# Kernel tuning notes

Measured on AMD Instinct MI355X. Metric: run time of the kernel, lower is better.

The kernel has to match this reference:

```python
import jax, jax.numpy as jnp
import numpy as np

N = 100000      # entities per graph
DIM = 128       # embedding / GAT dim
NHEADS = 2
NLAYER = 2
DH = DIM // NHEADS
DEG = 16        # avg in-degree
B = 4096        # alignment batch
ALPHA = 0.2     # LeakyReLU slope


def _make_edges(k):
    # random sources, uniform in-degree DEG per destination, plus self-loops
    src = jax.random.randint(k, (N * DEG,), 0, N)
    dst = jnp.repeat(jnp.arange(N), DEG)
    loop = jnp.arange(N)
    return jnp.stack([jnp.concatenate([src, loop]),
                      jnp.concatenate([dst, loop])]).astype(jnp.int32)


def setup_inputs() -> dict:
    key = jax.random.key(0)
    ks = jax.random.split(key, 9)
    emb_sr = jax.random.normal(ks[0], (N, DIM), jnp.float32) * 0.1
    emb_tg = jax.random.normal(ks[1], (N, DIM), jnp.float32) * 0.1
    edges_sr = _make_edges(ks[2])
    edges_tg = _make_edges(ks[3])
    Ws = jax.random.normal(ks[4], (NLAYER, NHEADS, DIM, DH), jnp.float32) / np.float32(np.sqrt(DIM))
    a_src = jax.random.normal(ks[5], (NLAYER, NHEADS, DH), jnp.float32) * 0.1
    a_dst = jax.random.normal(ks[6], (NLAYER, NHEADS, DH), jnp.float32) * 0.1
    sr_data = jax.random.randint(ks[7], (B,), 0, N)
    tg_data = jax.random.randint(ks[8], (B,), 0, N)
    return {"emb_sr": emb_sr, "emb_tg": emb_tg, "Ws": Ws, "a_src": a_src,
            "a_dst": a_dst, "edges_sr": edges_sr, "edges_tg": edges_tg,
            "sr_data": sr_data, "tg_data": tg_data}


def _gat(x, edges, Ws, a_src, a_dst):
    src, dst = edges[0], edges[1]
    for l in range(NLAYER):
        h = jnp.einsum('nd,hde->nhe', x, Ws[l])              # [N,H,DH]
        es = jnp.einsum('nhe,he->nh', h, a_src[l])           # [N,H]
        ed = jnp.einsum('nhe,he->nh', h, a_dst[l])           # [N,H]
        e = jax.nn.leaky_relu(es[src] + ed[dst], ALPHA)      # [E,H]
        m = jax.ops.segment_max(e, dst, num_segments=N)      # per-dst softmax
        w = jnp.exp(e - m[dst])
        denom = jax.ops.segment_sum(w, dst, num_segments=N)
        coef = w / (denom[dst] + 1e-16)                      # [E,H]
        out = jax.ops.segment_sum(coef[:, :, None] * h[src], dst, num_segments=N)
        out = out.reshape(N, NHEADS * DH)                    # concat heads
        x = jax.nn.elu(out) if l < NLAYER - 1 else out
    return x


def reference(emb_sr, emb_tg, Ws, a_src, a_dst, edges_sr, edges_tg, sr_data, tg_data):
    g_sr = _gat(emb_sr, edges_sr, Ws, a_src, a_dst)
    g_tg = _gat(emb_tg, edges_tg, Ws, a_src, a_dst)
    return g_sr[sr_data], g_tg[tg_data]
```

## Files before the change

kernel.cpp:

```cpp
#include <hip/hip_runtime.h>
#include <math.h>


#define N_NODES 100000
#define DIM     128
#define DH      64
#define DEG     16
#define BATCH   4096

typedef unsigned int   uint32;
typedef unsigned short u16;

typedef __attribute__((ext_vector_type(8))) short bf16x8;
typedef __attribute__((ext_vector_type(4))) float f32x4;

static __device__ __forceinline__ u16 bf16rne(float a) {
    uint32 ua = __float_as_uint(a);
    ua = (ua + 0x7FFFu + ((ua >> 16) & 1u)) >> 16;
    return (u16)ua;
}
static __device__ __forceinline__ uint32 bf2pack(float a, float b) {
    uint32 ua = __float_as_uint(a), ub = __float_as_uint(b);
    ua = (ua + 0x7FFFu + ((ua >> 16) & 1u)) >> 16;
    ub = (ub + 0x7FFFu + ((ub >> 16) & 1u)) >> 16;
    return (ub << 16) | (ua & 0xFFFFu);
}

__global__ void wfrag_init(const float* __restrict__ Ws, u16* __restrict__ wfrag) {
    const int l = blockIdx.x;
    for (int i = threadIdx.x; i < 16384; i += 256) {
        const int j = i & 7, lane = (i >> 3) & 63, nt = (i >> 9) & 7, ks = i >> 12;
        const int d = ks * 32 + (lane >> 4) * 8 + j;
        const int c = nt * 16 + (lane & 15);
        const float v = Ws[(size_t)(((l * 2 + (c >> 6)) * DIM) + d) * DH + (c & 63)];
        wfrag[l * 16384 + i] = bf16rne(v);
    }
}

template <bool BF16IN>
__global__ __launch_bounds__(256) void gat_transform_mfma(
    const void* __restrict__ xa, const void* __restrict__ xb,
    const u16* __restrict__ wfrag,
    const float* __restrict__ a_src,
    const float* __restrict__ a_dst,
    u16* __restrict__ hb,
    float* __restrict__ es,
    float* __restrict__ ed)
{
    __shared__ u16 xsh[64][136];

    const int g = blockIdx.y;
    const size_t row0 = (size_t)blockIdx.x * 64;
    const int t = threadIdx.x;

    if (BF16IN) {
        const u16* __restrict__ x = (const u16*)(g ? xb : xa);
        #pragma unroll
        for (int i = 0; i < 4; ++i) {
            const int c = i * 256 + t;
            const int r = c >> 4, col = (c & 15) * 8;
            const size_t gr = row0 + r;
            uint4 v = make_uint4(0u, 0u, 0u, 0u);
            if (gr < N_NODES) v = *(const uint4*)(x + gr * DIM + col);
            *(uint4*)&xsh[r][col] = v;
        }
    } else {
        const float* __restrict__ x = (const float*)(g ? xb : xa);
        #pragma unroll
        for (int i = 0; i < 8; ++i) {
            const int c = i * 256 + t;
            const int r = c >> 5, col = (c & 31) * 4;
            const size_t gr = row0 + r;
            float4 v = make_float4(0.f, 0.f, 0.f, 0.f);
            if (gr < N_NODES) v = *(const float4*)(x + gr * DIM + col);
            uint2 pk; pk.x = bf2pack(v.x, v.y); pk.y = bf2pack(v.z, v.w);
            *(uint2*)&xsh[r][col] = pk;
        }
    }
    __syncthreads();

    const int w = t >> 6, l = t & 63;
    const int wrow = w * 16;
    const int cl = l & 15, kg = l >> 4;

    f32x4 acc[8];
    #pragma unroll
    for (int nt = 0; nt < 8; ++nt) acc[nt] = (f32x4){0.f, 0.f, 0.f, 0.f};

    #pragma unroll
    for (int ks = 0; ks < 4; ++ks) {
        const bf16x8 a = *(const bf16x8*)&xsh[wrow + cl][ks * 32 + kg * 8];
        const u16* wp = wfrag + ks * 4096 + l * 8;
        #pragma unroll
        for (int nt = 0; nt < 8; ++nt) {
            const bf16x8 b = *(const bf16x8*)(wp + nt * 512);
            acc[nt] = __builtin_amdgcn_mfma_f32_16x16x32_bf16(a, b, acc[nt], 0, 0, 0);
        }
    }

    float av0[4], av1[4], dv0[4], dv1[4];
    #pragma unroll
    for (int nt = 0; nt < 4; ++nt) {
        av0[nt] = a_src[nt * 16 + cl];
        av1[nt] = a_src[DH + nt * 16 + cl];
        dv0[nt] = a_dst[nt * 16 + cl];
        dv1[nt] = a_dst[DH + nt * 16 + cl];
    }
    float pe0[4] = {0,0,0,0}, pe1[4] = {0,0,0,0};
    float pd0[4] = {0,0,0,0}, pd1[4] = {0,0,0,0};
    #pragma unroll
    for (int r = 0; r < 4; ++r)
        #pragma unroll
        for (int nt = 0; nt < 4; ++nt) {
            pe0[r] = fmaf(acc[nt][r],     av0[nt], pe0[r]);
            pd0[r] = fmaf(acc[nt][r],     dv0[nt], pd0[r]);
            pe1[r] = fmaf(acc[nt + 4][r], av1[nt], pe1[r]);
            pd1[r] = fmaf(acc[nt + 4][r], dv1[nt], pd1[r]);
        }
    #pragma unroll
    for (int msk = 1; msk < 16; msk <<= 1)
        #pragma unroll
        for (int r = 0; r < 4; ++r) {
            pe0[r] += __shfl_xor(pe0[r], msk, 64);
            pe1[r] += __shfl_xor(pe1[r], msk, 64);
            pd0[r] += __shfl_xor(pd0[r], msk, 64);
            pd1[r] += __shfl_xor(pd1[r], msk, 64);
        }
    if (cl == 0) {
        #pragma unroll
        for (int r = 0; r < 4; ++r) {
            const size_t gr = row0 + wrow + kg * 4 + r;
            if (gr < N_NODES) {
                const size_t o = ((size_t)g * N_NODES + gr) * 2;
                es[o] = pe0[r]; es[o + 1] = pe1[r];
                ed[o] = pd0[r]; ed[o + 1] = pd1[r];
            }
        }
    }

    __syncthreads();
    #pragma unroll
    for (int nt = 0; nt < 8; ++nt)
        #pragma unroll
        for (int r = 0; r < 4; ++r)
            xsh[wrow + kg * 4 + r][nt * 16 + cl] = bf16rne(acc[nt][r]);
    __syncthreads();
    #pragma unroll
    for (int i = 0; i < 4; ++i) {
        const int c = i * 256 + t;
        const int r = c >> 4, col = (c & 15) * 8;
        const size_t gr = row0 + r;
        if (gr < N_NODES)
            *(uint4*)(hb + ((size_t)g * N_NODES + gr) * DIM + col) = *(const uint4*)&xsh[r][col];
    }
}

template <bool FINAL>
__global__ __launch_bounds__(256) void gat_aggregate(
    const int* __restrict__ edges_a, const int* __restrict__ edges_b,
    const u16* __restrict__ hb, const float* __restrict__ es,
    const float* __restrict__ ed,
    const int* __restrict__ idx_a, const int* __restrict__ idx_b,
    void* __restrict__ out, int count)
{
    const int g   = blockIdx.y;
    const int wid = blockIdx.x * 4 + (threadIdx.x >> 6);
    if (wid >= count) return;
    const int lane = threadIdx.x & 63;
    const int head = lane >> 5;

    const int n = FINAL ? (g ? idx_b[wid] : idx_a[wid]) : wid;
    const int* __restrict__ edges = g ? edges_b : edges_a;
    const u16* __restrict__ hg   = hb + (size_t)g * N_NODES * DIM;
    const float* __restrict__ esg = es + (size_t)g * N_NODES * 2;

    const float edn = ed[((size_t)g * N_NODES + n) * 2 + head];

    int s[17];
    const int4* ep = (const int4*)(edges + (size_t)n * DEG);
    int4 q0 = ep[0], q1 = ep[1], q2 = ep[2], q3 = ep[3];
    s[0]=q0.x;  s[1]=q0.y;  s[2]=q0.z;  s[3]=q0.w;
    s[4]=q1.x;  s[5]=q1.y;  s[6]=q1.z;  s[7]=q1.w;
    s[8]=q2.x;  s[9]=q2.y;  s[10]=q2.z; s[11]=q2.w;
    s[12]=q3.x; s[13]=q3.y; s[14]=q3.z; s[15]=q3.w;
    s[16]=n;

    float w[17];
    float m = -1e30f;
    #pragma unroll
    for (int j = 0; j < 17; ++j) {
        float v = esg[s[j] * 2 + head] + edn;
        v = (v >= 0.f) ? v : 0.2f * v;
        w[j] = v;
        m = fmaxf(m, v);
    }
    float denom = 0.f;
    #pragma unroll
    for (int j = 0; j < 17; ++j) { w[j] = __expf(w[j] - m); denom += w[j]; }
    const float inv = 1.f / (denom + 1e-16f);

    float2 acc = make_float2(0.f, 0.f);
    #pragma unroll
    for (int j = 0; j < 17; ++j) {
        const uint32 u = *(const uint32*)(hg + (size_t)s[j] * DIM + lane * 2);
        const float hx = __uint_as_float(u << 16);
        const float hy = __uint_as_float(u & 0xFFFF0000u);
        acc.x = fmaf(w[j], hx, acc.x);
        acc.y = fmaf(w[j], hy, acc.y);
    }
    acc.x *= inv; acc.y *= inv;

    if (FINAL) {
        float* o = (float*)out + ((size_t)g * BATCH + wid) * DIM + lane * 2;
        *(float2*)o = acc;
    } else {
        acc.x = (acc.x > 0.f) ? acc.x : (__expf(acc.x) - 1.f);
        acc.y = (acc.y > 0.f) ? acc.y : (__expf(acc.y) - 1.f);
        u16* o = (u16*)out + ((size_t)g * N_NODES + n) * DIM + lane * 2;
        *(uint32*)o = bf2pack(acc.x, acc.y);
    }
}

extern "C" void kernel_launch(void* const* d_in, const int* in_sizes, int n_in,
                              void* d_out, int out_size, void* d_ws, size_t ws_size,
                              hipStream_t stream)
{
    const float* emb_sr = (const float*)d_in[0];
    const float* emb_tg = (const float*)d_in[1];
    const float* Ws     = (const float*)d_in[2];
    const float* a_src  = (const float*)d_in[3];
    const float* a_dst  = (const float*)d_in[4];
    const int*   edg_sr = (const int*)d_in[5];
    const int*   edg_tg = (const int*)d_in[6];
    const int*   sr_idx = (const int*)d_in[7];
    const int*   tg_idx = (const int*)d_in[8];

    u16*   hb    = (u16*)d_ws;
    u16*   x1b   = hb + (size_t)2 * N_NODES * DIM;
    float* es    = (float*)(x1b + (size_t)2 * N_NODES * DIM);
    float* ed    = es + (size_t)2 * N_NODES * 2;
    u16*   wfrag = (u16*)(ed + (size_t)2 * N_NODES * 2);

    const dim3 tgrd((N_NODES + 63) / 64, 2);
    const dim3 agrd(N_NODES / 4, 2);

    wfrag_init<<<2, 256, 0, stream>>>(Ws, wfrag);

    gat_transform_mfma<false><<<tgrd, 256, 0, stream>>>(
        emb_sr, emb_tg, wfrag, a_src, a_dst, hb, es, ed);
    gat_aggregate<false><<<agrd, 256, 0, stream>>>(
        edg_sr, edg_tg, hb, es, ed, nullptr, nullptr, x1b, N_NODES);

    gat_transform_mfma<true><<<tgrd, 256, 0, stream>>>(
        x1b, x1b + (size_t)N_NODES * DIM, wfrag + 16384,
        a_src + 2 * DH, a_dst + 2 * DH, hb, es, ed);
    gat_aggregate<true><<<dim3(BATCH / 4, 2), 256, 0, stream>>>(
        edg_sr, edg_tg, hb, es, ed, sr_idx, tg_idx, d_out, BATCH);
}
```

Baseline: 345.4 us.

## Fuse layer-1 aggregation with layer-2 MFMA transform via shared memory tile

The layer-1 neighbour aggregation (softmax plus ELU) now runs inside the layer-2 transform kernel. Each block aggregates its 64 destination rows into shared memory as bf16 and then runs the MFMA projection on them. This drops one launch and the global write and read of the intermediate x1 activations. Separate h, es and ed buffers per layer avoid overwriting data that other blocks are still reading. In exchange, each wave aggregates 16 rows one after another, which means fewer waves in flight to hide gather latency, and the aggregation uses one 256-thread block per 64 rows instead of one wave per row.

```diff
diff --git a/kernel.cpp b/kernel.cpp
--- a/kernel.cpp
+++ b/kernel.cpp
@@ -37,48 +37,12 @@
     }
 }
 
-template <bool BF16IN>
-__global__ __launch_bounds__(256) void gat_transform_mfma(
-    const void* __restrict__ xa, const void* __restrict__ xb,
-    const u16* __restrict__ wfrag,
-    const float* __restrict__ a_src,
-    const float* __restrict__ a_dst,
-    u16* __restrict__ hb,
-    float* __restrict__ es,
-    float* __restrict__ ed)
-{
-    __shared__ u16 xsh[64][136];
-
-    const int g = blockIdx.y;
-    const size_t row0 = (size_t)blockIdx.x * 64;
-    const int t = threadIdx.x;
-
-    if (BF16IN) {
-        const u16* __restrict__ x = (const u16*)(g ? xb : xa);
-        #pragma unroll
-        for (int i = 0; i < 4; ++i) {
-            const int c = i * 256 + t;
-            const int r = c >> 4, col = (c & 15) * 8;
-            const size_t gr = row0 + r;
-            uint4 v = make_uint4(0u, 0u, 0u, 0u);
-            if (gr < N_NODES) v = *(const uint4*)(x + gr * DIM + col);
-            *(uint4*)&xsh[r][col] = v;
-        }
-    } else {
-        const float* __restrict__ x = (const float*)(g ? xb : xa);
-        #pragma unroll
-        for (int i = 0; i < 8; ++i) {
-            const int c = i * 256 + t;
-            const int r = c >> 5, col = (c & 31) * 4;
-            const size_t gr = row0 + r;
-            float4 v = make_float4(0.f, 0.f, 0.f, 0.f);
-            if (gr < N_NODES) v = *(const float4*)(x + gr * DIM + col);
-            uint2 pk; pk.x = bf2pack(v.x, v.y); pk.y = bf2pack(v.z, v.w);
-            *(uint2*)&xsh[r][col] = pk;
-        }
-    }
-    __syncthreads();
-
+static __device__ __forceinline__ void mfma_tile_body(
+    u16 (*xsh)[136], int t, int g, size_t row0,
+    const u16* __restrict__ wfrag, const float* __restrict__ a_src,
+    const float* __restrict__ a_dst, u16* __restrict__ hb,
+    float* __restrict__ es, float* __restrict__ ed)
+{
     const int w = t >> 6, l = t & 63;
     const int wrow = w * 16;
     const int cl = l & 15, kg = l >> 4;
@@ -155,21 +119,113 @@
     }
 }
 
-template <bool FINAL>
-__global__ __launch_bounds__(256) void gat_aggregate(
+__global__ __launch_bounds__(256) void gat_transform_mfma(
+    const float* __restrict__ xa, const float* __restrict__ xb,
+    const u16* __restrict__ wfrag,
+    const float* __restrict__ a_src, const float* __restrict__ a_dst,
+    u16* __restrict__ hb, float* __restrict__ es, float* __restrict__ ed)
+{
+    __shared__ u16 xsh[64][136];
+    const int g = blockIdx.y;
+    const size_t row0 = (size_t)blockIdx.x * 64;
+    const int t = threadIdx.x;
+
+    const float* __restrict__ x = (const float*)(g ? xb : xa);
+    #pragma unroll
+    for (int i = 0; i < 8; ++i) {
+        const int c = i * 256 + t;
+        const int r = c >> 5, col = (c & 31) * 4;
+        const size_t gr = row0 + r;
+        float4 v = make_float4(0.f, 0.f, 0.f, 0.f);
+        if (gr < N_NODES) v = *(const float4*)(x + gr * DIM + col);
+        uint2 pk; pk.x = bf2pack(v.x, v.y); pk.y = bf2pack(v.z, v.w);
+        *(uint2*)&xsh[r][col] = pk;
+    }
+    __syncthreads();
+    mfma_tile_body(xsh, t, g, row0, wfrag, a_src, a_dst, hb, es, ed);
+}
+
+__global__ __launch_bounds__(256) void gat_fused_agg_transform(
+    const int* __restrict__ edges_a, const int* __restrict__ edges_b,
+    const u16* __restrict__ h0, const float* __restrict__ es0,
+    const float* __restrict__ ed0,
+    const u16* __restrict__ wfrag,
+    const float* __restrict__ a_src, const float* __restrict__ a_dst,
+    u16* __restrict__ h1, float* __restrict__ es1, float* __restrict__ ed1)
+{
+    __shared__ u16 xsh[64][136];
+    const int g = blockIdx.y;
+    const int t = threadIdx.x;
+    const int w = t >> 6, lane = t & 63;
+    const int head = lane >> 5;
+    const size_t dst0 = (size_t)blockIdx.x * 64;
+
+    const int* __restrict__ edges = g ? edges_b : edges_a;
+    const u16* __restrict__ hg    = h0  + (size_t)g * N_NODES * DIM;
+    const float* __restrict__ esg = es0 + (size_t)g * N_NODES * 2;
+    const float* __restrict__ edg = ed0 + (size_t)g * N_NODES * 2;
+
+    for (int i = 0; i < 16; ++i) {
+        const int r = w * 16 + i;
+        const size_t n = dst0 + r;
+        uint32 pk = 0u;
+        if (n < N_NODES) {
+            int s[17];
+            const int4* ep = (const int4*)(edges + n * DEG);
+            int4 q0 = ep[0], q1 = ep[1], q2 = ep[2], q3 = ep[3];
+            s[0]=q0.x;  s[1]=q0.y;  s[2]=q0.z;  s[3]=q0.w;
+            s[4]=q1.x;  s[5]=q1.y;  s[6]=q1.z;  s[7]=q1.w;
+            s[8]=q2.x;  s[9]=q2.y;  s[10]=q2.z; s[11]=q2.w;
+            s[12]=q3.x; s[13]=q3.y; s[14]=q3.z; s[15]=q3.w;
+            s[16]=(int)n;
+
+            const float edn = edg[n * 2 + head];
+            float wgt[17];
+            float m = -1e30f;
+            #pragma unroll
+            for (int j = 0; j < 17; ++j) {
+                float v = esg[s[j] * 2 + head] + edn;
+                v = (v >= 0.f) ? v : 0.2f * v;
+                wgt[j] = v;
+                m = fmaxf(m, v);
+            }
+            float denom = 0.f;
+            #pragma unroll
+            for (int j = 0; j < 17; ++j) { wgt[j] = __expf(wgt[j] - m); denom += wgt[j]; }
+            const float inv = 1.f / (denom + 1e-16f);
+
+            float2 acc = make_float2(0.f, 0.f);
+            #pragma unroll
+            for (int j = 0; j < 17; ++j) {
+                const uint32 u = *(const uint32*)(hg + (size_t)s[j] * DIM + lane * 2);
+                acc.x = fmaf(wgt[j], __uint_as_float(u << 16), acc.x);
+                acc.y = fmaf(wgt[j], __uint_as_float(u & 0xFFFF0000u), acc.y);
+            }
+            acc.x *= inv; acc.y *= inv;
+            acc.x = (acc.x > 0.f) ? acc.x : (__expf(acc.x) - 1.f);
+            acc.y = (acc.y > 0.f) ? acc.y : (__expf(acc.y) - 1.f);
+            pk = bf2pack(acc.x, acc.y);
+        }
+        *(uint32*)&xsh[r][lane * 2] = pk;
+    }
+    __syncthreads();
+    mfma_tile_body(xsh, t, g, dst0, wfrag, a_src, a_dst, h1, es1, ed1);
+}
+
+__global__ __launch_bounds__(256) void gat_aggregate_final(
     const int* __restrict__ edges_a, const int* __restrict__ edges_b,
     const u16* __restrict__ hb, const float* __restrict__ es,
     const float* __restrict__ ed,
     const int* __restrict__ idx_a, const int* __restrict__ idx_b,
-    void* __restrict__ out, int count)
+    float* __restrict__ out)
 {
     const int g   = blockIdx.y;
     const int wid = blockIdx.x * 4 + (threadIdx.x >> 6);
-    if (wid >= count) return;
+    if (wid >= BATCH) return;
     const int lane = threadIdx.x & 63;
     const int head = lane >> 5;
 
-    const int n = FINAL ? (g ? idx_b[wid] : idx_a[wid]) : wid;
+    const int n = g ? idx_b[wid] : idx_a[wid];
     const int* __restrict__ edges = g ? edges_b : edges_a;
     const u16* __restrict__ hg   = hb + (size_t)g * N_NODES * DIM;
     const float* __restrict__ esg = es + (size_t)g * N_NODES * 2;
@@ -185,40 +241,31 @@
     s[12]=q3.x; s[13]=q3.y; s[14]=q3.z; s[15]=q3.w;
     s[16]=n;
 
-    float w[17];
+    float wgt[17];
     float m = -1e30f;
     #pragma unroll
     for (int j = 0; j < 17; ++j) {
         float v = esg[s[j] * 2 + head] + edn;
         v = (v >= 0.f) ? v : 0.2f * v;
-        w[j] = v;
+        wgt[j] = v;
         m = fmaxf(m, v);
     }
     float denom = 0.f;
     #pragma unroll
-    for (int j = 0; j < 17; ++j) { w[j] = __expf(w[j] - m); denom += w[j]; }
+    for (int j = 0; j < 17; ++j) { wgt[j] = __expf(wgt[j] - m); denom += wgt[j]; }
     const float inv = 1.f / (denom + 1e-16f);
 
     float2 acc = make_float2(0.f, 0.f);
     #pragma unroll
     for (int j = 0; j < 17; ++j) {
         const uint32 u = *(const uint32*)(hg + (size_t)s[j] * DIM + lane * 2);
-        const float hx = __uint_as_float(u << 16);
-        const float hy = __uint_as_float(u & 0xFFFF0000u);
-        acc.x = fmaf(w[j], hx, acc.x);
-        acc.y = fmaf(w[j], hy, acc.y);
+        acc.x = fmaf(wgt[j], __uint_as_float(u << 16), acc.x);
+        acc.y = fmaf(wgt[j], __uint_as_float(u & 0xFFFF0000u), acc.y);
     }
     acc.x *= inv; acc.y *= inv;
 
-    if (FINAL) {
-        float* o = (float*)out + ((size_t)g * BATCH + wid) * DIM + lane * 2;
-        *(float2*)o = acc;
-    } else {
-        acc.x = (acc.x > 0.f) ? acc.x : (__expf(acc.x) - 1.f);
-        acc.y = (acc.y > 0.f) ? acc.y : (__expf(acc.y) - 1.f);
-        u16* o = (u16*)out + ((size_t)g * N_NODES + n) * DIM + lane * 2;
-        *(uint32*)o = bf2pack(acc.x, acc.y);
-    }
+    float* o = out + ((size_t)g * BATCH + wid) * DIM + lane * 2;
+    *(float2*)o = acc;
 }
 
 extern "C" void kernel_launch(void* const* d_in, const int* in_sizes, int n_in,
@@ -235,25 +282,25 @@
     const int*   sr_idx = (const int*)d_in[7];
     const int*   tg_idx = (const int*)d_in[8];
 
-    u16*   hb    = (u16*)d_ws;
-    u16*   x1b   = hb + (size_t)2 * N_NODES * DIM;
-    float* es    = (float*)(x1b + (size_t)2 * N_NODES * DIM);
-    float* ed    = es + (size_t)2 * N_NODES * 2;
-    u16*   wfrag = (u16*)(ed + (size_t)2 * N_NODES * 2);
+    u16*   h0    = (u16*)d_ws;
+    u16*   h1    = h0 + (size_t)2 * N_NODES * DIM;
+    float* es0   = (float*)(h1 + (size_t)2 * N_NODES * DIM);
+    float* ed0   = es0 + (size_t)2 * N_NODES * 2;
+    float* es1   = ed0 + (size_t)2 * N_NODES * 2;
+    float* ed1   = es1 + (size_t)2 * N_NODES * 2;
+    u16*   wfrag = (u16*)(ed1 + (size_t)2 * N_NODES * 2);
 
     const dim3 tgrd((N_NODES + 63) / 64, 2);
-    const dim3 agrd(N_NODES / 4, 2);
 
     wfrag_init<<<2, 256, 0, stream>>>(Ws, wfrag);
 
-    gat_transform_mfma<false><<<tgrd, 256, 0, stream>>>(
-        emb_sr, emb_tg, wfrag, a_src, a_dst, hb, es, ed);
-    gat_aggregate<false><<<agrd, 256, 0, stream>>>(
-        edg_sr, edg_tg, hb, es, ed, nullptr, nullptr, x1b, N_NODES);
-
-    gat_transform_mfma<true><<<tgrd, 256, 0, stream>>>(
-        x1b, x1b + (size_t)N_NODES * DIM, wfrag + 16384,
-        a_src + 2 * DH, a_dst + 2 * DH, hb, es, ed);
-    gat_aggregate<true><<<dim3(BATCH / 4, 2), 256, 0, stream>>>(
-        edg_sr, edg_tg, hb, es, ed, sr_idx, tg_idx, d_out, BATCH);
-}
+    gat_transform_mfma<<<tgrd, 256, 0, stream>>>(
+        emb_sr, emb_tg, wfrag, a_src, a_dst, h0, es0, ed0);
+
+    gat_fused_agg_transform<<<tgrd, 256, 0, stream>>>(
+        edg_sr, edg_tg, h0, es0, ed0, wfrag + 16384,
+        a_src + 2 * DH, a_dst + 2 * DH, h1, es1, ed1);
+
+    gat_aggregate_final<<<dim3(BATCH / 4, 2), 256, 0, stream>>>(
+        edg_sr, edg_tg, h1, es1, ed1, sr_idx, tg_idx, (float*)d_out);
+}
```

Measured after the change: 358.0 us. +3.7%, slower.
